# Kernel optimization log

Measured on AMD Instinct MI355X. Metric: run time of the kernel, lower is better.

Reference implementation:

```python
import jax, jax.numpy as jnp
import numpy as np

WIN = (7, 7)          # window_size (M, M)
DIM = 128             # C
HEADS = 4
B = 64                # images
NW = 64               # windows per image
NG = WIN[0] * WIN[1]  # 49 tokens per window
NT = 3136             # total patches per image (56x56)


def _relative_position_index(wh, ww):
    # Faithful to the TF code (default 'xy' meshgrid ordering, global token at (0,0))
    coords = np.stack(np.meshgrid(np.arange(wh), np.arange(ww)))        # (2, ww, wh)
    flat = coords.reshape(2, wh * ww)                                    # (2, M^2)
    flat1 = np.concatenate([flat, np.array([[0], [0]])], axis=1)         # (2, M^2+1)
    rel = flat[:, :, None] - flat1[:, None, :]                           # (2, M^2, M^2+1)
    rel = rel.transpose(1, 2, 0).astype(np.int32)
    rel[:, :, 0] += wh - 1
    rel[:, :, 1] += ww - 1
    rel[:, :, 0] *= 2 * ww - 1
    return rel.sum(-1)                                                   # (M^2, M^2+1)


def setup_inputs() -> dict:
    key = jax.random.key(0)
    ks = jax.random.split(key, 9)
    C, H = DIM, HEADS
    B_ = B * NW
    table_sz = (2 * WIN[0] - 1) * (2 * WIN[1] - 1)  # 169
    return {
        "x": jax.random.normal(ks[0], (B_, NG, C), jnp.float32),
        "xtotal": jax.random.normal(ks[1], (B, NT, C), jnp.float32),
        "xavg": jax.random.normal(ks[2], (B, 1, C), jnp.float32),
        "mask": jnp.zeros((NW, NG, NG + 1), jnp.float32),
        "W_q": jax.random.normal(ks[3], (C, C), jnp.float32) * (C ** -0.5),
        "b_q": jax.random.normal(ks[4], (C,), jnp.float32) * 0.02,
        "W_kv": jax.random.normal(ks[5], (C, 2 * C), jnp.float32) * (C ** -0.5),
        "b_kv": jax.random.normal(ks[6], (2 * C,), jnp.float32) * 0.02,
        "bias_table": jax.random.normal(ks[7], (table_sz, H), jnp.float32) * 0.02,
        "rel_idx": jnp.asarray(_relative_position_index(*WIN), jnp.int32),
    }


def reference(x, xtotal, xavg, mask, W_q, b_q, W_kv, b_kv, bias_table, rel_idx):
    B_, NGl, C = x.shape
    Bl = xavg.shape[0]
    H = bias_table.shape[1]
    d = C // H
    scale = d ** -0.5
    N = NGl + 1

    # window path: concat repeated global token, project kv / q
    xavgR = jnp.repeat(xavg, B_ // Bl, axis=0)               # (B_, 1, C)
    x_c = jnp.concatenate([x, xavgR], axis=1)                # (B_, N, C)
    kv = (x_c @ W_kv + b_kv).reshape(B_, N, 2, H, d).transpose(2, 0, 3, 1, 4)
    k, v = kv[0], kv[1]                                      # (B_, H, N, d)
    q = ((x @ W_q + b_q).reshape(B_, NGl, H, d).transpose(0, 2, 1, 3)) * scale

    attn = jnp.einsum('bhnd,bhmd->bhnm', q, k)               # (B_, H, NG, N)
    bias = bias_table[rel_idx.reshape(-1)].reshape(NGl, N, H).transpose(2, 0, 1)
    attn = attn + bias[None]
    nW = mask.shape[0]
    attn = attn.reshape(B_ // nW, nW, H, NGl, N) + mask[None, :, None]
    attn = jax.nn.softmax(attn.reshape(B_, H, NGl, N), axis=-1)
    x_out = jnp.einsum('bhnm,bhmd->bhnd', attn, v).transpose(0, 2, 1, 3).reshape(B_, NGl, C)

    # global path: q_avg (NOT scaled in the original), attends over all patches
    Nt = xtotal.shape[1]
    kvg = (xtotal @ W_kv + b_kv).reshape(Bl, Nt, 2, H, d).transpose(2, 0, 3, 1, 4)
    kg, vg = kvg[0], kvg[1]                                  # (B, H, Nt, d)
    q_avg = (xavg @ W_q + b_q).reshape(Bl, 1, H, d).transpose(0, 2, 1, 3)
    attng = jax.nn.softmax(jnp.einsum('bhqd,bhmd->bhqm', q_avg, kg), axis=-1)
    xavg_out = jnp.einsum('bhqm,bhmd->bhqd', attng, vg).transpose(0, 2, 1, 3).reshape(Bl, 1, C)
    return x_out, xavg_out
```

## Files before the change

### kernel.cpp

```cpp
#include <hip/hip_runtime.h>
#include <hip/hip_bf16.h>

#define NB_  4096
#define NG_  49
#define NC_  128
#define NH_  4
#define DH_  32
#define NN_  50
#define NIMG 64
#define NT_  3136
#define NCHK 8
#define CROWS 392
#define SCALE_ 0.17677669529663687f

#define WT_LO_OFF 49152
#define BM_OFF    98304
#define FBASE  573440
#define U_F    (FBASE)
#define CST_F  (FBASE + 32768)
#define WACC_F (FBASE + 33024)
#define SUM_F  (FBASE + 65792)
#define CNT_F  (FBASE + 66048)

typedef unsigned short u16;
typedef unsigned int   u32;
typedef __attribute__((ext_vector_type(8))) short bf16x8;
typedef __attribute__((ext_vector_type(4))) float f32x4;

__device__ __forceinline__ float b2f(u16 u) {
    union { u32 i; float f; } v; v.i = ((u32)u) << 16; return v.f;
}
__device__ __forceinline__ u16 f2b(float f) {
    union { float f; u32 i; } v; v.f = f;
    u32 x = v.i;
    return (u16)((x + 0x7fffu + ((x >> 16) & 1u)) >> 16);
}
__device__ __forceinline__ u32 pk2(float a, float b) {
    union { __hip_bfloat162 h2; u32 u; } v;
    v.h2 = __float22bfloat162_rn(make_float2(a, b));
    return v.u;
}

extern "C" __global__ __launch_bounds__(256)
void prep_kernel(const float* __restrict__ Wq, const float* __restrict__ Wkv,
                 const float* __restrict__ btab, const int* __restrict__ ridx,
                 const float* __restrict__ mask, const float* __restrict__ xavg,
                 const float* __restrict__ bq, const float* __restrict__ bkv,
                 u16* __restrict__ ws)
{
    __shared__ int   ridxS[NG_ * NN_];
    __shared__ float btabS[169 * NH_];
    __shared__ float xavgS[NC_];
    __shared__ float qaS[NC_];
    const int t = threadIdx.x, b = blockIdx.x;
    if (b < 24) {
        const int tn = b, kt = t >> 6, lane = t & 63;
        const int j  = tn * 16 + (lane & 15);
        const int k0 = kt * 32 + (lane >> 4) * 8;
        const float qs = (j < 128) ? SCALE_ : 1.f;
        u32 hi[4], lo[4];
        #pragma unroll
        for (int p = 0; p < 4; ++p) {
            const int k = k0 + 2 * p;
            float w0 = ((j < 128) ? Wq[(size_t)k * 128 + j]       : Wkv[(size_t)k * 256 + (j - 128)]) * qs;
            float w1 = ((j < 128) ? Wq[(size_t)(k + 1) * 128 + j] : Wkv[(size_t)(k + 1) * 256 + (j - 128)]) * qs;
            u16 h0 = f2b(w0), h1 = f2b(w1);
            hi[p] = (u32)h0 | ((u32)h1 << 16);
            lo[p] = (u32)f2b(w0 - b2f(h0)) | ((u32)f2b(w1 - b2f(h1)) << 16);
        }
        const size_t fo = ((size_t)(tn * 4 + kt) * 64 + lane) * 8;
        *(uint4*)(ws + fo)             = make_uint4(hi[0], hi[1], hi[2], hi[3]);
        *(uint4*)(ws + WT_LO_OFF + fo) = make_uint4(lo[0], lo[1], lo[2], lo[3]);
    } else if (b < 88) {
        const int wx = b - 24;
        for (int i = t; i < NG_ * NN_; i += 256) ridxS[i] = ridx[i];
        for (int i = t; i < 169 * NH_; i += 256) btabS[i] = btab[i];
        __syncthreads();
        for (int i = t; i < NH_ * 16 * 64; i += 256) {
            const int lane = i & 63, tile = (i >> 6) & 15, h = i >> 10;
            const int n  = 16 * (tile >> 2) + (lane & 15);
            const int m0 = 16 * (tile & 3) + 4 * (lane >> 4);
            u16 vv[4];
            #pragma unroll
            for (int e = 0; e < 4; ++e) {
                const int m = m0 + e;
                float val = -1e30f;
                if (n < NG_ && m < NN_)
                    val = btabS[ridxS[n * NN_ + m] * NH_ + h] + mask[((size_t)wx * NG_ + n) * NN_ + m];
                vv[e] = f2b(val);
            }
            u32* dst = (u32*)(ws + BM_OFF + ((size_t)((wx * NH_ + h) * 16 + tile) * 64 + lane) * 4);
            dst[0] = (u32)vv[0] | ((u32)vv[1] << 16);
            dst[1] = (u32)vv[2] | ((u32)vv[3] << 16);
        }
    } else {
        const int img = b - 88;
        float* wsF = (float*)ws;
        if (t < NC_) xavgS[t] = xavg[img * NC_ + t];
        __syncthreads();
        if (t < NC_) {
            float acc = bq[t];
            for (int c = 0; c < NC_; ++c) acc += xavgS[c] * Wq[c * NC_ + t];
            qaS[t] = acc;
        }
        __syncthreads();
        if (t < NC_) {
            const int c = t;
            const float* wr = Wkv + (size_t)c * 256;
            #pragma unroll
            for (int h = 0; h < NH_; ++h) {
                float acc = 0.f;
                #pragma unroll
                for (int j = 0; j < 32; ++j) acc += wr[h * 32 + j] * qaS[h * 32 + j];
                wsF[U_F + img * 512 + h * 128 + c] = acc;
            }
            #pragma unroll
            for (int h = 0; h < NH_; ++h) wsF[WACC_F + img * 512 + h * 128 + t] = 0.f;
        } else if (t < NC_ + NH_) {
            const int h = t - NC_;
            float acc = 0.f;
            for (int j = 0; j < 32; ++j) acc += qaS[h * 32 + j] * bkv[h * 32 + j];
            wsF[CST_F + img * 4 + h] = acc;
            wsF[SUM_F + img * 4 + h] = 0.f;
        } else if (t == NC_ + NH_) {
            ((int*)wsF)[CNT_F + img] = 0;
        }
    }
}

struct WinShared {
    u16 q[64][128];
    u16 k[64][128];
    u16 buf[64 * 128];
};
struct ChunkShared {
    float waccS[4][4][128];
    float esumS[4][4];
    float sumS[4];
    int   flagS;
};
union SMem { WinShared w; ChunkShared c; };

extern "C" __global__ __launch_bounds__(256, 4)
void wa2_kernel(const float* __restrict__ x, const float* __restrict__ xtotal,
                const float* __restrict__ xavg,
                const float* __restrict__ Wq, const float* __restrict__ bq,
                const float* __restrict__ Wkv, const float* __restrict__ bkv,
                float* __restrict__ out, u16* __restrict__ ws)
{
    __shared__ SMem sm;
    const int t = threadIdx.x;
    const int blk = blockIdx.x;
    const int lane = t & 63, wv = t >> 6;

    if (blk >= NIMG * NCHK) {
        WinShared& S = sm.w;
        const int wb   = blk - NIMG * NCHK;
        const int img  = wb >> 6;
        const int widx = wb & 63;
        const int l15  = lane & 15, g = lane >> 4;

        {
            u16* xc = S.buf;
            const float2* xr = (const float2*)(x + (size_t)wb * (NG_ * NC_));
            for (int i = t; i < NG_ * 64; i += 256) {
                const int row = i >> 6, cp = i & 63;
                float2 xv = xr[i];
                *(u32*)&xc[row * 128 + ((2 * cp) ^ ((row & 7) << 3))] = pk2(xv.x, xv.y);
            }
            if (t < 64) {
                float2 av = ((const float2*)(xavg + (size_t)img * NC_))[t];
                *(u32*)&xc[49 * 128 + ((2 * t) ^ 8)] = pk2(av.x, av.y);
            }
            for (int i = t; i < 14 * 64; i += 256) {
                const int row = 50 + (i >> 6), cp = i & 63;
                *(u32*)&xc[row * 128 + ((2 * cp) ^ ((row & 7) << 3))] = 0u;
            }
        }
        __syncthreads();

        const int sw = (l15 & 7) << 3;

        bf16x8 a[4][4];
        #pragma unroll
        for (int tm = 0; tm < 4; ++tm)
            #pragma unroll
            for (int kt = 0; kt < 4; ++kt)
                a[tm][kt] = *(const bf16x8*)&S.buf[(16 * tm + l15) * 128 + ((32 * kt + 8 * g) ^ sw)];
        __syncthreads();

        {
            u16* vT = S.buf;
            for (int i = 0; i < 6; ++i) {
                const int tn = 6 * wv + i;
                const int jc = tn * 16 + l15;
                const float bias = (jc < 128) ? bq[jc] * SCALE_ : bkv[jc - 128];
                f32x4 acc[4];
                #pragma unroll
                for (int tm = 0; tm < 4; ++tm) acc[tm] = (f32x4){bias, bias, bias, bias};
                #pragma unroll
                for (int kt = 0; kt < 4; ++kt) {
                    const size_t fo = ((size_t)(tn * 4 + kt) * 64 + lane) * 8;
                    bf16x8 bh = *(const bf16x8*)(ws + fo);
                    bf16x8 bl = *(const bf16x8*)(ws + WT_LO_OFF + fo);
                    #pragma unroll
                    for (int tm = 0; tm < 4; ++tm) {
                        acc[tm] = __builtin_amdgcn_mfma_f32_16x16x32_bf16(a[tm][kt], bh, acc[tm], 0, 0, 0);
                        acc[tm] = __builtin_amdgcn_mfma_f32_16x16x32_bf16(a[tm][kt], bl, acc[tm], 0, 0, 0);
                    }
                }
                #pragma unroll
                for (int tm = 0; tm < 4; ++tm) {
                    #pragma unroll
                    for (int rp = 0; rp < 2; ++rp) {
                        const int r0 = 16 * tm + 4 * g + 2 * rp;
                        const u32 p = pk2(acc[tm][2 * rp], acc[tm][2 * rp + 1]);
                        if (jc < 128) {
                            S.q[r0][jc ^ ((r0 & 7) << 3)]           = (u16)p;
                            S.q[r0 + 1][jc ^ (((r0 + 1) & 7) << 3)] = (u16)(p >> 16);
                        } else if (jc < 256) {
                            const int c = jc - 128;
                            S.k[r0][c ^ ((r0 & 7) << 3)]           = (u16)p;
                            S.k[r0 + 1][c ^ (((r0 + 1) & 7) << 3)] = (u16)(p >> 16);
                        } else {
                            const int c = jc - 256, swc = (c & 7) << 3;
                            vT[c * 64 + (r0 ^ swc)]       = (u16)p;
                            vT[c * 64 + ((r0 + 1) ^ swc)] = (u16)(p >> 16);
                        }
                    }
                }
            }
        }
        __syncthreads();

        {
            const int h = wv;
            const u16* vT = S.buf;
            bf16x8 ka[4], qb[4];
            #pragma unroll
            for (int tk = 0; tk < 4; ++tk)
                ka[tk] = *(const bf16x8*)&S.k[16 * tk + l15][(32 * h + 8 * g) ^ sw];
            #pragma unroll
            for (int tq = 0; tq < 4; ++tq)
                qb[tq] = *(const bf16x8*)&S.q[16 * tq + l15][(32 * h + 8 * g) ^ sw];

            const u16* bmb = ws + BM_OFF + (size_t)(widx * NH_ + h) * 4096;
            f32x4 s[4][4];
            #pragma unroll
            for (int tq = 0; tq < 4; ++tq)
                #pragma unroll
                for (int tk = 0; tk < 4; ++tk) {
                    uint2 bm = *(const uint2*)(bmb + ((size_t)(tq * 4 + tk) * 64 + lane) * 4);
                    f32x4 c0;
                    c0[0] = b2f((u16)bm.x); c0[1] = b2f((u16)(bm.x >> 16));
                    c0[2] = b2f((u16)bm.y); c0[3] = b2f((u16)(bm.y >> 16));
                    s[tk][tq] = __builtin_amdgcn_mfma_f32_16x16x32_bf16(ka[tk], qb[tq], c0, 0, 0, 0);
                }

            float inv[4];
            #pragma unroll
            for (int tq = 0; tq < 4; ++tq) {
                float m = s[0][tq][0];
                #pragma unroll
                for (int tk = 0; tk < 4; ++tk)
                    #pragma unroll
                    for (int r = 0; r < 4; ++r) m = fmaxf(m, s[tk][tq][r]);
                m = fmaxf(m, __shfl_xor(m, 16));
                m = fmaxf(m, __shfl_xor(m, 32));
                float sum = 0.f;
                #pragma unroll
                for (int tk = 0; tk < 4; ++tk)
                    #pragma unroll
                    for (int r = 0; r < 4; ++r) {
                        float e = __expf(s[tk][tq][r] - m);
                        s[tk][tq][r] = e;
                        sum += e;
                    }
                sum += __shfl_xor(sum, 16);
                sum += __shfl_xor(sum, 32);
                inv[tq] = 1.f / sum;
            }

            bf16x8 pa[4][2];
            #pragma unroll
            for (int tq = 0; tq < 4; ++tq) {
                const float iv = inv[tq];
                #pragma unroll
                for (int kt = 0; kt < 2; ++kt) {
                    union { u32 u[4]; bf16x8 v; } P;
                    P.u[0] = pk2(s[2 * kt][tq][0] * iv, s[2 * kt][tq][1] * iv);
                    P.u[1] = pk2(s[2 * kt][tq][2] * iv, s[2 * kt][tq][3] * iv);
                    P.u[2] = pk2(s[2 * kt + 1][tq][0] * iv, s[2 * kt + 1][tq][1] * iv);
                    P.u[3] = pk2(s[2 * kt + 1][tq][2] * iv, s[2 * kt + 1][tq][3] * iv);
                    pa[tq][kt] = P.v;
                }
            }
            bf16x8 vb[2][2];
            #pragma unroll
            for (int tn = 0; tn < 2; ++tn) {
                const int c = 32 * h + 16 * tn + l15;
                const int swv = (c & 7) << 3;
                #pragma unroll
                for (int kt = 0; kt < 2; ++kt) {
                    union { uint2 u2[2]; bf16x8 v; } B;
                    B.u2[0] = *(const uint2*)&vT[c * 64 + ((32 * kt + 4 * g) ^ swv)];
                    B.u2[1] = *(const uint2*)&vT[c * 64 + ((32 * kt + 16 + 4 * g) ^ swv)];
                    vb[kt][tn] = B.v;
                }
            }
            #pragma unroll
            for (int tq = 0; tq < 4; ++tq)
                #pragma unroll
                for (int tn = 0; tn < 2; ++tn) {
                    f32x4 acc = {0.f, 0.f, 0.f, 0.f};
                    acc = __builtin_amdgcn_mfma_f32_16x16x32_bf16(pa[tq][0], vb[0][tn], acc, 0, 0, 0);
                    acc = __builtin_amdgcn_mfma_f32_16x16x32_bf16(pa[tq][1], vb[1][tn], acc, 0, 0, 0);
                    #pragma unroll
                    for (int r = 0; r < 4; ++r) {
                        const int row = 16 * tq + 4 * g + r;
                        if (row < NG_)
                            out[(size_t)wb * (NG_ * NC_) + (size_t)row * NC_ + 32 * h + 16 * tn + l15] = acc[r];
                    }
                }
        }
    } else {
        ChunkShared& S = sm.c;
        float* wsF = (float*)ws;
        const int img = blk >> 3, ch = blk & 7;
        const int c0 = (lane & 31) * 4, roff = lane >> 5;

        float4 uR[NH_]; float cstR[NH_];
        #pragma unroll
        for (int h = 0; h < NH_; ++h) {
            uR[h]  = *(const float4*)&wsF[U_F + img * 512 + h * 128 + c0];
            cstR[h] = wsF[CST_F + img * 4 + h];
        }

        float wacc[NH_][4] = {};
        float esum[NH_] = {0.f, 0.f, 0.f, 0.f};
        const float* xb = xtotal + ((size_t)img * NT_ + ch * CROWS) * NC_;
        for (int it = 0; it < CROWS / 8; ++it) {
            const int m = it * 8 + wv * 2 + roff;
            float4 xv = *(const float4*)&xb[(size_t)m * NC_ + c0];
            float s[NH_];
            #pragma unroll
            for (int h = 0; h < NH_; ++h)
                s[h] = xv.x * uR[h].x + xv.y * uR[h].y + xv.z * uR[h].z + xv.w * uR[h].w;
            #pragma unroll
            for (int off = 1; off < 32; off <<= 1) {
                #pragma unroll
                for (int h = 0; h < NH_; ++h) s[h] += __shfl_xor(s[h], off);
            }
            #pragma unroll
            for (int h = 0; h < NH_; ++h) {
                const float e = __expf(s[h] + cstR[h]);
                wacc[h][0] += e * xv.x; wacc[h][1] += e * xv.y;
                wacc[h][2] += e * xv.z; wacc[h][3] += e * xv.w;
                if ((lane & 31) == 0) esum[h] += e;
            }
        }

        #pragma unroll
        for (int h = 0; h < NH_; ++h) {
            #pragma unroll
            for (int i = 0; i < 4; ++i) wacc[h][i] += __shfl_xor(wacc[h][i], 32);
            esum[h] += __shfl_xor(esum[h], 32);
        }
        if (lane < 32) {
            #pragma unroll
            for (int h = 0; h < NH_; ++h)
                #pragma unroll
                for (int i = 0; i < 4; ++i) S.waccS[wv][h][c0 + i] = wacc[h][i];
            if (lane == 0) {
                #pragma unroll
                for (int h = 0; h < NH_; ++h) S.esumS[wv][h] = esum[h];
            }
        }
        __syncthreads();
        if (t < NC_) {
            #pragma unroll
            for (int h = 0; h < NH_; ++h) {
                float v = S.waccS[0][h][t] + S.waccS[1][h][t] + S.waccS[2][h][t] + S.waccS[3][h][t];
                atomicAdd(&wsF[WACC_F + img * 512 + h * 128 + t], v);
            }
        } else if (t < NC_ + NH_) {
            const int h = t - NC_;
            atomicAdd(&wsF[SUM_F + img * 4 + h],
                      S.esumS[0][h] + S.esumS[1][h] + S.esumS[2][h] + S.esumS[3][h]);
        }
        __threadfence();
        __syncthreads();
        if (t == 0) S.flagS = atomicAdd(&((int*)wsF)[CNT_F + img], 1);
        __syncthreads();
        if (S.flagS == NCHK - 1) {
            float* wS = &S.waccS[0][0][0];
            for (int i = t; i < 512; i += 256)
                wS[i] = atomicAdd(&wsF[WACC_F + img * 512 + i], 0.f);
            if (t < NH_) S.sumS[t] = atomicAdd(&wsF[SUM_F + img * 4 + t], 0.f);
            __syncthreads();
            if (t < NC_) {
                const int h = t >> 5;
                const float inv = 1.f / S.sumS[h];
                float acc = bkv[NC_ + t];
                for (int c = 0; c < NC_; ++c)
                    acc += (wS[h * 128 + c] * inv) * Wkv[(size_t)c * 256 + NC_ + t];
                out[(size_t)NB_ * (NG_ * NC_) + img * NC_ + t] = acc;
            }
        }
    }
}

extern "C" void kernel_launch(void* const* d_in, const int* in_sizes, int n_in,
                              void* d_out, int out_size, void* d_ws, size_t ws_size,
                              hipStream_t stream) {
    const float* x      = (const float*)d_in[0];
    const float* xtotal = (const float*)d_in[1];
    const float* xavg   = (const float*)d_in[2];
    const float* mask   = (const float*)d_in[3];
    const float* Wq     = (const float*)d_in[4];
    const float* bq     = (const float*)d_in[5];
    const float* Wkv    = (const float*)d_in[6];
    const float* bkv    = (const float*)d_in[7];
    const float* btab   = (const float*)d_in[8];
    const int*   ridx   = (const int*)d_in[9];
    float* outp = (float*)d_out;
    u16*   ws   = (u16*)d_ws;
    (void)in_sizes; (void)n_in; (void)out_size; (void)ws_size;

    prep_kernel<<<152, 256, 0, stream>>>(Wq, Wkv, btab, ridx, mask, xavg, bq, bkv, ws);
    wa2_kernel<<<NIMG * NCHK + NB_, 256, 0, stream>>>(x, xtotal, xavg, Wq, bq,
                                                      Wkv, bkv, outp, ws);
}
```

Measured before the change: 442.5 us.

## Keep window attention in registers per head, dropping shared-memory staging

The window path no longer stages x, Q, K and transposed V through shared memory. Each wave now owns one head and loads x straight from global into bf16 MFMA fragments. It computes its own Q, K and V projections with reordered weight fragments so the outputs land directly in the operand layouts the attention MFMAs need, and processes query tiles one at a time. This removes about 48KB of LDS, several block barriers and the LDS round-trips. In exchange every wave re-reads all of x from global (4x redundant reads), and register pressure rises, so launch bounds drop from 4 to 3 waves.

```diff
diff --git a/kernel.cpp b/kernel.cpp
--- a/kernel.cpp
+++ b/kernel.cpp
@@ -54,21 +54,27 @@
     __shared__ float qaS[NC_];
     const int t = threadIdx.x, b = blockIdx.x;
     if (b < 24) {
-        const int tn = b, kt = t >> 6, lane = t & 63;
-        const int j  = tn * 16 + (lane & 15);
-        const int k0 = kt * 32 + (lane >> 4) * 8;
-        const float qs = (j < 128) ? SCALE_ : 1.f;
+        const int fp  = b * 4 + (t >> 6);
+        const int lane = t & 63, l15 = lane & 15, g = lane >> 4;
+        const int kt = fp & 3, rest = fp >> 2, jt = rest & 1, hty = rest >> 1;
+        const int ty = hty % 3, hh = hty / 3;
+        const int jc = 32 * hh + 16 * jt + l15;
+        const float* src; int stride; float qs = 1.f;
+        if (ty == 0)      { src = Wq  + jc;       stride = NC_;     qs = SCALE_; }
+        else if (ty == 1) { src = Wkv + jc;       stride = 2 * NC_; }
+        else              { src = Wkv + NC_ + jc; stride = 2 * NC_; }
+        const int c0 = 32 * kt + 8 * g;
         u32 hi[4], lo[4];
         #pragma unroll
         for (int p = 0; p < 4; ++p) {
-            const int k = k0 + 2 * p;
-            float w0 = ((j < 128) ? Wq[(size_t)k * 128 + j]       : Wkv[(size_t)k * 256 + (j - 128)]) * qs;
-            float w1 = ((j < 128) ? Wq[(size_t)(k + 1) * 128 + j] : Wkv[(size_t)(k + 1) * 256 + (j - 128)]) * qs;
+            const int c = c0 + 2 * p;
+            float w0 = src[(size_t)c * stride] * qs;
+            float w1 = src[(size_t)(c + 1) * stride] * qs;
             u16 h0 = f2b(w0), h1 = f2b(w1);
             hi[p] = (u32)h0 | ((u32)h1 << 16);
             lo[p] = (u32)f2b(w0 - b2f(h0)) | ((u32)f2b(w1 - b2f(h1)) << 16);
         }
-        const size_t fo = ((size_t)(tn * 4 + kt) * 64 + lane) * 8;
+        const size_t fo = ((size_t)fp * 64 + lane) * 8;
         *(uint4*)(ws + fo)             = make_uint4(hi[0], hi[1], hi[2], hi[3]);
         *(uint4*)(ws + WT_LO_OFF + fo) = make_uint4(lo[0], lo[1], lo[2], lo[3]);
     } else if (b < 88) {
@@ -128,203 +134,188 @@
     }
 }
 
-struct WinShared {
-    u16 q[64][128];
-    u16 k[64][128];
-    u16 buf[64 * 128];
-};
 struct ChunkShared {
     float waccS[4][4][128];
     float esumS[4][4];
     float sumS[4];
     int   flagS;
 };
-union SMem { WinShared w; ChunkShared c; };
-
-extern "C" __global__ __launch_bounds__(256, 4)
+
+extern "C" __global__ __launch_bounds__(256, 3)
 void wa2_kernel(const float* __restrict__ x, const float* __restrict__ xtotal,
                 const float* __restrict__ xavg,
                 const float* __restrict__ Wq, const float* __restrict__ bq,
                 const float* __restrict__ Wkv, const float* __restrict__ bkv,
                 float* __restrict__ out, u16* __restrict__ ws)
 {
-    __shared__ SMem sm;
+    __shared__ ChunkShared smc;
     const int t = threadIdx.x;
     const int blk = blockIdx.x;
     const int lane = t & 63, wv = t >> 6;
 
     if (blk >= NIMG * NCHK) {
-        WinShared& S = sm.w;
         const int wb   = blk - NIMG * NCHK;
         const int img  = wb >> 6;
         const int widx = wb & 63;
-        const int l15  = lane & 15, g = lane >> 4;
-
+        const int h = wv, l15 = lane & 15, g = lane >> 4;
+
+        bf16x8 xf[4][4];
         {
-            u16* xc = S.buf;
-            const float2* xr = (const float2*)(x + (size_t)wb * (NG_ * NC_));
-            for (int i = t; i < NG_ * 64; i += 256) {
-                const int row = i >> 6, cp = i & 63;
-                float2 xv = xr[i];
-                *(u32*)&xc[row * 128 + ((2 * cp) ^ ((row & 7) << 3))] = pk2(xv.x, xv.y);
-            }
-            if (t < 64) {
-                float2 av = ((const float2*)(xavg + (size_t)img * NC_))[t];
-                *(u32*)&xc[49 * 128 + ((2 * t) ^ 8)] = pk2(av.x, av.y);
-            }
-            for (int i = t; i < 14 * 64; i += 256) {
-                const int row = 50 + (i >> 6), cp = i & 63;
-                *(u32*)&xc[row * 128 + ((2 * cp) ^ ((row & 7) << 3))] = 0u;
-            }
-        }
-        __syncthreads();
-
-        const int sw = (l15 & 7) << 3;
-
-        bf16x8 a[4][4];
+            const float* xbase = x + (size_t)wb * (NG_ * NC_);
+            #pragma unroll
+            for (int rt = 0; rt < 4; ++rt) {
+                const int row = 16 * rt + l15;
+                const float* rp = (row < NG_) ? (xbase + (size_t)row * NC_)
+                                              : (xavg + (size_t)img * NC_);
+                const bool vld = (row <= NG_);
+                #pragma unroll
+                for (int kt = 0; kt < 4; ++kt) {
+                    float4 u0 = *(const float4*)(rp + 32 * kt + 8 * g);
+                    float4 u1 = *(const float4*)(rp + 32 * kt + 8 * g + 4);
+                    if (!vld) { u0 = make_float4(0.f,0.f,0.f,0.f); u1 = make_float4(0.f,0.f,0.f,0.f); }
+                    union { u32 w[4]; bf16x8 v; } F;
+                    F.w[0] = pk2(u0.x, u0.y); F.w[1] = pk2(u0.z, u0.w);
+                    F.w[2] = pk2(u1.x, u1.y); F.w[3] = pk2(u1.z, u1.w);
+                    xf[rt][kt] = F.v;
+                }
+            }
+        }
+
+        bf16x8 qf[4], kf[4];
         #pragma unroll
-        for (int tm = 0; tm < 4; ++tm)
-            #pragma unroll
-            for (int kt = 0; kt < 4; ++kt)
-                a[tm][kt] = *(const bf16x8*)&S.buf[(16 * tm + l15) * 128 + ((32 * kt + 8 * g) ^ sw)];
-        __syncthreads();
-
+        for (int ty = 0; ty < 2; ++ty) {
+            f32x4 acc[2][4];
+            #pragma unroll
+            for (int jt = 0; jt < 2; ++jt) {
+                f32x4 cin;
+                #pragma unroll
+                for (int r = 0; r < 4; ++r) {
+                    const int j = 32 * h + 16 * jt + 4 * g + r;
+                    cin[r] = (ty == 0) ? bq[j] * SCALE_ : bkv[j];
+                }
+                #pragma unroll
+                for (int rt = 0; rt < 4; ++rt) acc[jt][rt] = cin;
+            }
+            #pragma unroll
+            for (int kt = 0; kt < 4; ++kt) {
+                const int fpb = ((h * 3 + ty) * 2) * 4 + kt;
+                const bf16x8 wh0 = *(const bf16x8*)(ws + ((size_t)fpb * 64 + lane) * 8);
+                const bf16x8 wl0 = *(const bf16x8*)(ws + WT_LO_OFF + ((size_t)fpb * 64 + lane) * 8);
+                const bf16x8 wh1 = *(const bf16x8*)(ws + ((size_t)(fpb + 4) * 64 + lane) * 8);
+                const bf16x8 wl1 = *(const bf16x8*)(ws + WT_LO_OFF + ((size_t)(fpb + 4) * 64 + lane) * 8);
+                #pragma unroll
+                for (int rt = 0; rt < 4; ++rt) {
+                    acc[0][rt] = __builtin_amdgcn_mfma_f32_16x16x32_bf16(wh0, xf[rt][kt], acc[0][rt], 0, 0, 0);
+                    acc[0][rt] = __builtin_amdgcn_mfma_f32_16x16x32_bf16(wl0, xf[rt][kt], acc[0][rt], 0, 0, 0);
+                    acc[1][rt] = __builtin_amdgcn_mfma_f32_16x16x32_bf16(wh1, xf[rt][kt], acc[1][rt], 0, 0, 0);
+                    acc[1][rt] = __builtin_amdgcn_mfma_f32_16x16x32_bf16(wl1, xf[rt][kt], acc[1][rt], 0, 0, 0);
+                }
+            }
+            #pragma unroll
+            for (int rt = 0; rt < 4; ++rt) {
+                union { u32 w[4]; bf16x8 v; } F;
+                F.w[0] = pk2(acc[0][rt][0], acc[0][rt][1]);
+                F.w[1] = pk2(acc[0][rt][2], acc[0][rt][3]);
+                F.w[2] = pk2(acc[1][rt][0], acc[1][rt][1]);
+                F.w[3] = pk2(acc[1][rt][2], acc[1][rt][3]);
+                if (ty == 0) qf[rt] = F.v; else kf[rt] = F.v;
+            }
+        }
+
+        bf16x8 vbf[2][2];
         {
-            u16* vT = S.buf;
-            for (int i = 0; i < 6; ++i) {
-                const int tn = 6 * wv + i;
-                const int jc = tn * 16 + l15;
-                const float bias = (jc < 128) ? bq[jc] * SCALE_ : bkv[jc - 128];
-                f32x4 acc[4];
-                #pragma unroll
-                for (int tm = 0; tm < 4; ++tm) acc[tm] = (f32x4){bias, bias, bias, bias};
-                #pragma unroll
-                for (int kt = 0; kt < 4; ++kt) {
-                    const size_t fo = ((size_t)(tn * 4 + kt) * 64 + lane) * 8;
-                    bf16x8 bh = *(const bf16x8*)(ws + fo);
-                    bf16x8 bl = *(const bf16x8*)(ws + WT_LO_OFF + fo);
-                    #pragma unroll
-                    for (int tm = 0; tm < 4; ++tm) {
-                        acc[tm] = __builtin_amdgcn_mfma_f32_16x16x32_bf16(a[tm][kt], bh, acc[tm], 0, 0, 0);
-                        acc[tm] = __builtin_amdgcn_mfma_f32_16x16x32_bf16(a[tm][kt], bl, acc[tm], 0, 0, 0);
-                    }
-                }
+            f32x4 vacc[4][2];
+            #pragma unroll
+            for (int tn = 0; tn < 2; ++tn) {
+                const float bv = bkv[NC_ + 32 * h + 16 * tn + l15];
+                #pragma unroll
+                for (int tm = 0; tm < 4; ++tm) vacc[tm][tn] = (f32x4){bv, bv, bv, bv};
+            }
+            #pragma unroll
+            for (int kt = 0; kt < 4; ++kt) {
+                const int fpb = ((h * 3 + 2) * 2) * 4 + kt;
+                const bf16x8 wh0 = *(const bf16x8*)(ws + ((size_t)fpb * 64 + lane) * 8);
+                const bf16x8 wl0 = *(const bf16x8*)(ws + WT_LO_OFF + ((size_t)fpb * 64 + lane) * 8);
+                const bf16x8 wh1 = *(const bf16x8*)(ws + ((size_t)(fpb + 4) * 64 + lane) * 8);
+                const bf16x8 wl1 = *(const bf16x8*)(ws + WT_LO_OFF + ((size_t)(fpb + 4) * 64 + lane) * 8);
                 #pragma unroll
                 for (int tm = 0; tm < 4; ++tm) {
-                    #pragma unroll
-                    for (int rp = 0; rp < 2; ++rp) {
-                        const int r0 = 16 * tm + 4 * g + 2 * rp;
-                        const u32 p = pk2(acc[tm][2 * rp], acc[tm][2 * rp + 1]);
-                        if (jc < 128) {
-                            S.q[r0][jc ^ ((r0 & 7) << 3)]           = (u16)p;
-                            S.q[r0 + 1][jc ^ (((r0 + 1) & 7) << 3)] = (u16)(p >> 16);
-                        } else if (jc < 256) {
-                            const int c = jc - 128;
-                            S.k[r0][c ^ ((r0 & 7) << 3)]           = (u16)p;
-                            S.k[r0 + 1][c ^ (((r0 + 1) & 7) << 3)] = (u16)(p >> 16);
-                        } else {
-                            const int c = jc - 256, swc = (c & 7) << 3;
-                            vT[c * 64 + (r0 ^ swc)]       = (u16)p;
-                            vT[c * 64 + ((r0 + 1) ^ swc)] = (u16)(p >> 16);
-                        }
-                    }
-                }
-            }
-        }
-        __syncthreads();
-
-        {
-            const int h = wv;
-            const u16* vT = S.buf;
-            bf16x8 ka[4], qb[4];
+                    vacc[tm][0] = __builtin_amdgcn_mfma_f32_16x16x32_bf16(xf[tm][kt], wh0, vacc[tm][0], 0, 0, 0);
+                    vacc[tm][0] = __builtin_amdgcn_mfma_f32_16x16x32_bf16(xf[tm][kt], wl0, vacc[tm][0], 0, 0, 0);
+                    vacc[tm][1] = __builtin_amdgcn_mfma_f32_16x16x32_bf16(xf[tm][kt], wh1, vacc[tm][1], 0, 0, 0);
+                    vacc[tm][1] = __builtin_amdgcn_mfma_f32_16x16x32_bf16(xf[tm][kt], wl1, vacc[tm][1], 0, 0, 0);
+                }
+            }
+            #pragma unroll
+            for (int kt2 = 0; kt2 < 2; ++kt2)
+                #pragma unroll
+                for (int tn = 0; tn < 2; ++tn) {
+                    union { u32 w[4]; bf16x8 v; } F;
+                    F.w[0] = pk2(vacc[2 * kt2][tn][0], vacc[2 * kt2][tn][1]);
+                    F.w[1] = pk2(vacc[2 * kt2][tn][2], vacc[2 * kt2][tn][3]);
+                    F.w[2] = pk2(vacc[2 * kt2 + 1][tn][0], vacc[2 * kt2 + 1][tn][1]);
+                    F.w[3] = pk2(vacc[2 * kt2 + 1][tn][2], vacc[2 * kt2 + 1][tn][3]);
+                    vbf[kt2][tn] = F.v;
+                }
+        }
+
+        const u16* bmb = ws + BM_OFF + (size_t)(widx * NH_ + h) * 4096;
+        #pragma unroll
+        for (int tq = 0; tq < 4; ++tq) {
+            f32x4 s[4];
+            #pragma unroll
+            for (int tk = 0; tk < 4; ++tk) {
+                uint2 bm = *(const uint2*)(bmb + ((size_t)(tq * 4 + tk) * 64 + lane) * 4);
+                f32x4 c0;
+                c0[0] = b2f((u16)bm.x); c0[1] = b2f((u16)(bm.x >> 16));
+                c0[2] = b2f((u16)bm.y); c0[3] = b2f((u16)(bm.y >> 16));
+                s[tk] = __builtin_amdgcn_mfma_f32_16x16x32_bf16(kf[tk], qf[tq], c0, 0, 0, 0);
+            }
+            float mx = s[0][0];
             #pragma unroll
             for (int tk = 0; tk < 4; ++tk)
-                ka[tk] = *(const bf16x8*)&S.k[16 * tk + l15][(32 * h + 8 * g) ^ sw];
-            #pragma unroll
-            for (int tq = 0; tq < 4; ++tq)
-                qb[tq] = *(const bf16x8*)&S.q[16 * tq + l15][(32 * h + 8 * g) ^ sw];
-
-            const u16* bmb = ws + BM_OFF + (size_t)(widx * NH_ + h) * 4096;
-            f32x4 s[4][4];
-            #pragma unroll
-            for (int tq = 0; tq < 4; ++tq)
-                #pragma unroll
-                for (int tk = 0; tk < 4; ++tk) {
-                    uint2 bm = *(const uint2*)(bmb + ((size_t)(tq * 4 + tk) * 64 + lane) * 4);
-                    f32x4 c0;
-                    c0[0] = b2f((u16)bm.x); c0[1] = b2f((u16)(bm.x >> 16));
-                    c0[2] = b2f((u16)bm.y); c0[3] = b2f((u16)(bm.y >> 16));
-                    s[tk][tq] = __builtin_amdgcn_mfma_f32_16x16x32_bf16(ka[tk], qb[tq], c0, 0, 0, 0);
-                }
-
-            float inv[4];
-            #pragma unroll
-            for (int tq = 0; tq < 4; ++tq) {
-                float m = s[0][tq][0];
-                #pragma unroll
-                for (int tk = 0; tk < 4; ++tk)
-                    #pragma unroll
-                    for (int r = 0; r < 4; ++r) m = fmaxf(m, s[tk][tq][r]);
-                m = fmaxf(m, __shfl_xor(m, 16));
-                m = fmaxf(m, __shfl_xor(m, 32));
-                float sum = 0.f;
-                #pragma unroll
-                for (int tk = 0; tk < 4; ++tk)
-                    #pragma unroll
-                    for (int r = 0; r < 4; ++r) {
-                        float e = __expf(s[tk][tq][r] - m);
-                        s[tk][tq][r] = e;
-                        sum += e;
-                    }
-                sum += __shfl_xor(sum, 16);
-                sum += __shfl_xor(sum, 32);
-                inv[tq] = 1.f / sum;
-            }
-
-            bf16x8 pa[4][2];
-            #pragma unroll
-            for (int tq = 0; tq < 4; ++tq) {
-                const float iv = inv[tq];
-                #pragma unroll
-                for (int kt = 0; kt < 2; ++kt) {
-                    union { u32 u[4]; bf16x8 v; } P;
-                    P.u[0] = pk2(s[2 * kt][tq][0] * iv, s[2 * kt][tq][1] * iv);
-                    P.u[1] = pk2(s[2 * kt][tq][2] * iv, s[2 * kt][tq][3] * iv);
-                    P.u[2] = pk2(s[2 * kt + 1][tq][0] * iv, s[2 * kt + 1][tq][1] * iv);
-                    P.u[3] = pk2(s[2 * kt + 1][tq][2] * iv, s[2 * kt + 1][tq][3] * iv);
-                    pa[tq][kt] = P.v;
-                }
-            }
-            bf16x8 vb[2][2];
+                #pragma unroll
+                for (int r = 0; r < 4; ++r) mx = fmaxf(mx, s[tk][r]);
+            mx = fmaxf(mx, __shfl_xor(mx, 16));
+            mx = fmaxf(mx, __shfl_xor(mx, 32));
+            float sum = 0.f;
+            #pragma unroll
+            for (int tk = 0; tk < 4; ++tk)
+                #pragma unroll
+                for (int r = 0; r < 4; ++r) {
+                    float e = __expf(s[tk][r] - mx);
+                    s[tk][r] = e;
+                    sum += e;
+                }
+            sum += __shfl_xor(sum, 16);
+            sum += __shfl_xor(sum, 32);
+            const float inv = 1.f / sum;
+
+            bf16x8 pa[2];
+            #pragma unroll
+            for (int kt2 = 0; kt2 < 2; ++kt2) {
+                union { u32 w[4]; bf16x8 v; } P;
+                P.w[0] = pk2(s[2 * kt2][0] * inv, s[2 * kt2][1] * inv);
+                P.w[1] = pk2(s[2 * kt2][2] * inv, s[2 * kt2][3] * inv);
+                P.w[2] = pk2(s[2 * kt2 + 1][0] * inv, s[2 * kt2 + 1][1] * inv);
+                P.w[3] = pk2(s[2 * kt2 + 1][2] * inv, s[2 * kt2 + 1][3] * inv);
+                pa[kt2] = P.v;
+            }
             #pragma unroll
             for (int tn = 0; tn < 2; ++tn) {
-                const int c = 32 * h + 16 * tn + l15;
-                const int swv = (c & 7) << 3;
-                #pragma unroll
-                for (int kt = 0; kt < 2; ++kt) {
-                    union { uint2 u2[2]; bf16x8 v; } B;
-                    B.u2[0] = *(const uint2*)&vT[c * 64 + ((32 * kt + 4 * g) ^ swv)];
-                    B.u2[1] = *(const uint2*)&vT[c * 64 + ((32 * kt + 16 + 4 * g) ^ swv)];
-                    vb[kt][tn] = B.v;
-                }
-            }
-            #pragma unroll
-            for (int tq = 0; tq < 4; ++tq)
-                #pragma unroll
-                for (int tn = 0; tn < 2; ++tn) {
-                    f32x4 acc = {0.f, 0.f, 0.f, 0.f};
-                    acc = __builtin_amdgcn_mfma_f32_16x16x32_bf16(pa[tq][0], vb[0][tn], acc, 0, 0, 0);
-                    acc = __builtin_amdgcn_mfma_f32_16x16x32_bf16(pa[tq][1], vb[1][tn], acc, 0, 0, 0);
-                    #pragma unroll
-                    for (int r = 0; r < 4; ++r) {
-                        const int row = 16 * tq + 4 * g + r;
-                        if (row < NG_)
-                            out[(size_t)wb * (NG_ * NC_) + (size_t)row * NC_ + 32 * h + 16 * tn + l15] = acc[r];
-                    }
-                }
+                f32x4 o = {0.f, 0.f, 0.f, 0.f};
+                o = __builtin_amdgcn_mfma_f32_16x16x32_bf16(pa[0], vbf[0][tn], o, 0, 0, 0);
+                o = __builtin_amdgcn_mfma_f32_16x16x32_bf16(pa[1], vbf[1][tn], o, 0, 0, 0);
+                #pragma unroll
+                for (int r = 0; r < 4; ++r) {
+                    const int row = 16 * tq + 4 * g + r;
+                    if (row < NG_)
+                        out[(size_t)wb * (NG_ * NC_) + (size_t)row * NC_ + 32 * h + 16 * tn + l15] = o[r];
+                }
+            }
         }
     } else {
-        ChunkShared& S = sm.c;
+        ChunkShared& S = smc;
         float* wsF = (float*)ws;
         const int img = blk >> 3, ch = blk & 7;
         const int c0 = (lane & 31) * 4, roff = lane >> 5;
```

New measurement: 426.6 us. -3.6%, faster.
